# Kernel tuning notes

Measured on AMD Instinct MI355X. Metric: run time of the kernel, lower is better.

The kernel has to match this reference:

```python
import jax, jax.numpy as jnp
import numpy as np

N_NODES = 100000
N_GRAPHS = 64


def _gcn_norm(edge_index, num_nodes):
    # Add self-loops and compute symmetric normalization (PyG GCNConv gcn_norm).
    src = jnp.concatenate([edge_index[0], jnp.arange(num_nodes, dtype=edge_index.dtype)])
    dst = jnp.concatenate([edge_index[1], jnp.arange(num_nodes, dtype=edge_index.dtype)])
    deg = jax.ops.segment_sum(jnp.ones_like(dst, dtype=jnp.float32), dst, num_segments=num_nodes)
    dinv = jnp.where(deg > 0, jax.lax.rsqrt(deg), 0.0)
    norm = dinv[src] * dinv[dst]  # [E + N]
    return src, dst, norm


def _gcn_conv(x, src, dst, norm, W, b, num_nodes):
    h = x @ W                                   # [N, out]
    msg = h[src] * norm[:, None]                # gather + scale  [E+N, out]
    out = jax.ops.segment_sum(msg, dst, num_segments=num_nodes)  # scatter-add
    return out + b


def setup_inputs() -> dict:
    key = jax.random.key(0)
    ks = jax.random.split(key, 8)
    E = 1600000
    pos = jax.random.normal(ks[0], (N_NODES, 3), dtype=jnp.float32)
    edge_index = jax.random.randint(ks[1], (2, E), 0, N_NODES, dtype=jnp.int64)
    batch = jnp.sort(jax.random.randint(ks[2], (N_NODES,), 0, N_GRAPHS, dtype=jnp.int64))
    def glorot(k, shape):
        lim = np.sqrt(6.0 / (shape[0] + shape[1])).astype(np.float32)
        return jax.random.uniform(k, shape, dtype=jnp.float32, minval=-lim, maxval=lim)
    return {
        "pos": pos,
        "edge_index": edge_index,
        "batch": batch,
        "W1": glorot(ks[3], (3, 64)),  "b1": jnp.zeros((64,), jnp.float32),
        "W2": glorot(ks[4], (64, 64)), "b2": jnp.zeros((64,), jnp.float32),
        "W3": glorot(ks[5], (64, 24)), "b3": jnp.zeros((24,), jnp.float32),
    }


def reference(pos, edge_index, batch, W1, b1, W2, b2, W3, b3):
    src, dst, norm = _gcn_norm(edge_index, N_NODES)
    h = jax.nn.relu(_gcn_conv(pos, src, dst, norm, W1, b1, N_NODES))
    h = jax.nn.relu(_gcn_conv(h, src, dst, norm, W2, b2, N_NODES))
    y = _gcn_conv(h, src, dst, norm, W3, b3, N_NODES)  # [N, 24]
    # global_mean_pool over batch ids, then tanh
    sums = jax.ops.segment_sum(y, batch, num_segments=N_GRAPHS)          # [G, 24]
    counts = jax.ops.segment_sum(jnp.ones((N_NODES,), jnp.float32), batch, num_segments=N_GRAPHS)
    mean = sums / jnp.maximum(counts, 1.0)[:, None]
    return jnp.tanh(mean)
```

## Files before the change

kernel.cpp:

```cpp
#include <hip/hip_runtime.h>
#include <math.h>

#define NNODES 100000
#define NGRAPHS 64
#define NB 391
#define CAP 4608
#define NBLK3 1216


__device__ __forceinline__ unsigned int f2bf(float x) {
    union { float f; unsigned int u; } v;
    v.f = x;
    unsigned int r = v.u + 0x7FFFu + ((v.u >> 16) & 1u);
    return r >> 16;
}
__device__ __forceinline__ unsigned int pack2bf(float lo, float hi) {
    return f2bf(lo) | (f2bf(hi) << 16);
}
__device__ __forceinline__ float bflo(unsigned int u) {
    union { unsigned int u; float f; } v;
    v.u = u << 16;
    return v.f;
}
__device__ __forceinline__ float bfhi(unsigned int u) {
    union { unsigned int u; float f; } v;
    v.u = u & 0xFFFF0000u;
    return v.f;
}


__global__ void bucket_scatter(const int* __restrict__ src, const int* __restrict__ dst,
                               int* __restrict__ bCur, unsigned int* __restrict__ packed,
                               int E) {
    __shared__ int h[NB];
    __shared__ int cur[NB];
    for (int k = threadIdx.x; k < NB; k += 256) h[k] = 0;
    __syncthreads();
    int base = blockIdx.x * 2048 + threadIdx.x;
    int d[8], s[8], b[8];
#pragma unroll
    for (int k = 0; k < 8; ++k) {
        int e = base + k * 256;
        if (e < E) {
            d[k] = dst[e];
            s[k] = src[e];
            b[k] = d[k] >> 8;
            atomicAdd(&h[b[k]], 1);
        }
    }
    __syncthreads();
    for (int k = threadIdx.x; k < NB; k += 256) {
        int c = h[k];
        cur[k] = c ? atomicAdd(&bCur[k], c) : 0;
    }
    __syncthreads();
#pragma unroll
    for (int k = 0; k < 8; ++k) {
        int e = base + k * 256;
        if (e < E) {
            int pos = atomicAdd(&cur[b[k]], 1);
            if (pos < CAP)
                packed[(size_t)b[k] * CAP + pos] = ((unsigned int)(d[k] & 255) << 17) | (unsigned int)s[k];
        }
    }
}

__global__ void bucket_build(const unsigned int* __restrict__ packed, const int* __restrict__ bCur,
                             const int* __restrict__ batch, const float* __restrict__ pos,
                             int2* __restrict__ rowBE, int* __restrict__ col,
                             float* __restrict__ dinv, int2* __restrict__ dg,
                             float4* __restrict__ pos4, int N_) {
    __shared__ int cnt[256];
    __shared__ int bas[256];
    int tid = threadIdx.x;
    int b = blockIdx.x;
    int count = bCur[b];
    if (count > CAP) count = CAP;
    int beg = b * CAP;
    cnt[tid] = 0;
    __syncthreads();
    for (int k = beg + tid; k < beg + count; k += 256) atomicAdd(&cnt[packed[k] >> 17], 1);
    __syncthreads();
    int myCnt = cnt[tid];
    bas[tid] = myCnt;
    __syncthreads();
    for (int off = 1; off < 256; off <<= 1) {
        int v = (tid >= off) ? bas[tid - off] : 0;
        __syncthreads();
        bas[tid] += v;
        __syncthreads();
    }
    int excl = beg + ((tid > 0) ? bas[tid - 1] : 0);
    int node = (b << 8) + tid;
    if (node < N_) {
        rowBE[node] = make_int2(excl, excl + myCnt);
        float di = rsqrtf((float)myCnt + 1.0f);
        dinv[node] = di;
        dg[node] = make_int2(__float_as_int(di), batch[node]);
        pos4[node] = make_float4(pos[node * 3] * di, pos[node * 3 + 1] * di,
                                 pos[node * 3 + 2] * di, di);
    }
    __syncthreads();
    bas[tid] = excl;
    __syncthreads();
    for (int k = beg + tid; k < beg + count; k += 256) {
        unsigned int p = packed[k];
        int pos_ = atomicAdd(&bas[p >> 17], 1);
        col[pos_] = (int)(p & 0x1FFFFu);
    }
}


__global__ void mm12_gp(const float4* __restrict__ pos4, const int2* __restrict__ rowBE,
                        const int* __restrict__ col, const float* __restrict__ dinv,
                        const float* __restrict__ W1, const float* __restrict__ b1,
                        const float* __restrict__ W2, uint2* __restrict__ outb, int n) {
    __shared__ float4 part[256];
    __shared__ float4 ag[64];
    __shared__ float xs[64][65];
    __shared__ float4 ws[64 * 16];
    const int tid = threadIdx.x;
    const int rowBase = blockIdx.x * 64;
    const int r = tid >> 2, t4 = tid & 3;
    const int i = rowBase + r;

    float sx = 0, sy = 0, sz = 0, dival = 0;
    if (i < n) {
        int2 be = rowBE[i];
        float4 ps = pos4[i];
        dival = ps.w;
        if (t4 == 0) { sx = ps.x; sy = ps.y; sz = ps.z; }
        for (int j = be.x + t4; j < be.y; j += 4) {
            float4 v = pos4[col[j]];
            sx += v.x; sy += v.y; sz += v.z;
        }
    }
    part[tid] = make_float4(sx, sy, sz, dival);
    const float4* W24 = (const float4*)W2;
    for (int idx = tid; idx < 64 * 16; idx += 256) ws[idx] = W24[idx];
    __syncthreads();
    if (tid < 64) {
        float4 p0 = part[tid * 4], p1 = part[tid * 4 + 1];
        float4 p2 = part[tid * 4 + 2], p3 = part[tid * 4 + 3];
        ag[tid] = make_float4((p0.x + p1.x) + (p2.x + p3.x),
                              (p0.y + p1.y) + (p2.y + p3.y),
                              (p0.z + p1.z) + (p2.z + p3.z), p0.w);
    }
    __syncthreads();
    for (int idx = tid; idx < 64 * 64; idx += 256) {
        int rr = idx >> 6;
        int k = idx & 63;
        float4 a = ag[rr];
        float v = b1[k] + a.w * (a.x * W1[k] + a.y * W1[64 + k] + a.z * W1[128 + k]);
        xs[rr][k] = fmaxf(v, 0.0f);
    }
    __syncthreads();

    const int f4 = tid & 15;
    const int r0 = (tid >> 4) * 4;
    float4 a0 = make_float4(0, 0, 0, 0), a1 = a0, a2 = a0, a3 = a0;
#pragma unroll 4
    for (int k = 0; k < 64; ++k) {
        float4 wv = ws[k * 16 + f4];
        float xa = xs[r0 + 0][k];
        float xb = xs[r0 + 1][k];
        float xc = xs[r0 + 2][k];
        float xd = xs[r0 + 3][k];
        a0.x += wv.x * xa; a0.y += wv.y * xa; a0.z += wv.z * xa; a0.w += wv.w * xa;
        a1.x += wv.x * xb; a1.y += wv.y * xb; a1.z += wv.z * xb; a1.w += wv.w * xb;
        a2.x += wv.x * xc; a2.y += wv.y * xc; a2.z += wv.z * xc; a2.w += wv.w * xc;
        a3.x += wv.x * xd; a3.y += wv.y * xd; a3.z += wv.z * xd; a3.w += wv.w * xd;
    }
    int i0 = rowBase + r0;
    float d0 = (i0 + 0 < n) ? dinv[i0 + 0] : 1.0f;
    float d1 = (i0 + 1 < n) ? dinv[i0 + 1] : 1.0f;
    float d2 = (i0 + 2 < n) ? dinv[i0 + 2] : 1.0f;
    float d3 = (i0 + 3 < n) ? dinv[i0 + 3] : 1.0f;
    if (i0 + 0 < n)
        outb[(size_t)(i0 + 0) * 16 + f4] = make_uint2(pack2bf(a0.x * d0, a0.y * d0), pack2bf(a0.z * d0, a0.w * d0));
    if (i0 + 1 < n)
        outb[(size_t)(i0 + 1) * 16 + f4] = make_uint2(pack2bf(a1.x * d1, a1.y * d1), pack2bf(a1.z * d1, a1.w * d1));
    if (i0 + 2 < n)
        outb[(size_t)(i0 + 2) * 16 + f4] = make_uint2(pack2bf(a2.x * d2, a2.y * d2), pack2bf(a2.z * d2, a2.w * d2));
    if (i0 + 3 < n)
        outb[(size_t)(i0 + 3) * 16 + f4] = make_uint2(pack2bf(a3.x * d3, a3.y * d3), pack2bf(a3.z * d3, a3.w * d3));
}


__global__ void gather2_b16(const int2* __restrict__ rowBE, const int* __restrict__ col,
                            const uint4* __restrict__ h, const float* __restrict__ dinv,
                            const float* __restrict__ bias, uint4* __restrict__ outb, int n) {
    int t = blockIdx.x * blockDim.x + threadIdx.x;
    if (t >= n * 8) return;
    int i = t >> 3;
    int c8 = t & 7;
    float di = dinv[i];
    int2 be = rowBE[i];
    float acc[8];
    {
        uint4 sv = h[t];
        acc[0] = bflo(sv.x); acc[1] = bfhi(sv.x);
        acc[2] = bflo(sv.y); acc[3] = bfhi(sv.y);
        acc[4] = bflo(sv.z); acc[5] = bfhi(sv.z);
        acc[6] = bflo(sv.w); acc[7] = bfhi(sv.w);
    }
    int j = be.x;
    for (; j + 8 <= be.y; j += 8) {
        int s[8];
        uint4 v[8];
#pragma unroll
        for (int k = 0; k < 8; ++k) s[k] = col[j + k];
#pragma unroll
        for (int k = 0; k < 8; ++k) v[k] = h[(size_t)s[k] * 8 + c8];
#pragma unroll
        for (int k = 0; k < 8; ++k) {
            acc[0] += bflo(v[k].x); acc[1] += bfhi(v[k].x);
            acc[2] += bflo(v[k].y); acc[3] += bfhi(v[k].y);
            acc[4] += bflo(v[k].z); acc[5] += bfhi(v[k].z);
            acc[6] += bflo(v[k].w); acc[7] += bfhi(v[k].w);
        }
    }
    for (; j < be.y; ++j) {
        uint4 v = h[(size_t)col[j] * 8 + c8];
        acc[0] += bflo(v.x); acc[1] += bfhi(v.x);
        acc[2] += bflo(v.y); acc[3] += bfhi(v.y);
        acc[4] += bflo(v.z); acc[5] += bfhi(v.z);
        acc[6] += bflo(v.w); acc[7] += bfhi(v.w);
    }
    const float* bv = bias + c8 * 8;
#pragma unroll
    for (int k = 0; k < 8; ++k) acc[k] = fmaxf(acc[k] * di + bv[k], 0.0f);
    outb[t] = make_uint4(pack2bf(acc[0], acc[1]), pack2bf(acc[2], acc[3]),
                         pack2bf(acc[4], acc[5]), pack2bf(acc[6], acc[7]));
}


__global__ void mm3_b16(const uint4* __restrict__ xb, const float* __restrict__ W,
                        const float* __restrict__ dinv, uint2* __restrict__ outb, int n) {
    __shared__ float xs[128][65];
    __shared__ float4 ws[64 * 6];
    const int tid = threadIdx.x;
    const int rowBase = blockIdx.x * 128;

    for (int idx = tid; idx < 128 * 8; idx += 192) {
        int r = idx >> 3;
        int c8 = idx & 7;
        int gr = rowBase + r;
        uint4 v = (gr < n) ? xb[(size_t)gr * 8 + c8] : make_uint4(0, 0, 0, 0);
        float* xp = &xs[r][c8 * 8];
        xp[0] = bflo(v.x); xp[1] = bfhi(v.x);
        xp[2] = bflo(v.y); xp[3] = bfhi(v.y);
        xp[4] = bflo(v.z); xp[5] = bfhi(v.z);
        xp[6] = bflo(v.w); xp[7] = bfhi(v.w);
    }
    const float4* W4 = (const float4*)W;
    for (int idx = tid; idx < 64 * 6; idx += 192) ws[idx] = W4[idx];
    __syncthreads();

    const int f4 = tid % 6;
    const int r0 = (tid / 6) * 4;
    float4 a0 = make_float4(0, 0, 0, 0), a1 = a0, a2 = a0, a3 = a0;
#pragma unroll 4
    for (int k = 0; k < 64; ++k) {
        float4 wv = ws[k * 6 + f4];
        float xa = xs[r0 + 0][k];
        float xb_ = xs[r0 + 1][k];
        float xc = xs[r0 + 2][k];
        float xd = xs[r0 + 3][k];
        a0.x += wv.x * xa; a0.y += wv.y * xa; a0.z += wv.z * xa; a0.w += wv.w * xa;
        a1.x += wv.x * xb_; a1.y += wv.y * xb_; a1.z += wv.z * xb_; a1.w += wv.w * xb_;
        a2.x += wv.x * xc; a2.y += wv.y * xc; a2.z += wv.z * xc; a2.w += wv.w * xc;
        a3.x += wv.x * xd; a3.y += wv.y * xd; a3.z += wv.z * xd; a3.w += wv.w * xd;
    }
    int i0 = rowBase + r0;
    float d0 = (i0 + 0 < n) ? dinv[i0 + 0] : 1.0f;
    float d1 = (i0 + 1 < n) ? dinv[i0 + 1] : 1.0f;
    float d2 = (i0 + 2 < n) ? dinv[i0 + 2] : 1.0f;
    float d3 = (i0 + 3 < n) ? dinv[i0 + 3] : 1.0f;
    if (i0 + 0 < n)
        outb[(size_t)(i0 + 0) * 6 + f4] = make_uint2(pack2bf(a0.x * d0, a0.y * d0), pack2bf(a0.z * d0, a0.w * d0));
    if (i0 + 1 < n)
        outb[(size_t)(i0 + 1) * 6 + f4] = make_uint2(pack2bf(a1.x * d1, a1.y * d1), pack2bf(a1.z * d1, a1.w * d1));
    if (i0 + 2 < n)
        outb[(size_t)(i0 + 2) * 6 + f4] = make_uint2(pack2bf(a2.x * d2, a2.y * d2), pack2bf(a2.z * d2, a2.w * d2));
    if (i0 + 3 < n)
        outb[(size_t)(i0 + 3) * 6 + f4] = make_uint2(pack2bf(a3.x * d3, a3.y * d3), pack2bf(a3.z * d3, a3.w * d3));
}


__global__ void gather3_pool(const int2* __restrict__ rowBE, const int* __restrict__ col,
                             const uint4* __restrict__ y0, const int2* __restrict__ dg,
                             float* __restrict__ partials, float* __restrict__ cpart, int n) {
    __shared__ float lpool[NGRAPHS * 24];
    __shared__ float lcnt[NGRAPHS];
    for (int k = threadIdx.x; k < NGRAPHS * 24; k += 256) lpool[k] = 0.0f;
    for (int k = threadIdx.x; k < NGRAPHS; k += 256) lcnt[k] = 0.0f;
    __syncthreads();

    const int T = n * 6;
    const int stride = NBLK3 * 256;
    for (int t = blockIdx.x * 256 + threadIdx.x; t < T; t += stride) {
        int i = t / 6;
        int q = t - i * 6;
        int r = q >> 1;
        int half = q & 1;
        int2 wi = dg[i];
        float di = __int_as_float(wi.x);
        int g = wi.y;
        int2 be = rowBE[i];
        int mid = be.x + ((be.y - be.x + 1) >> 1);
        int a = half ? mid : be.x;
        int b = half ? be.y : mid;
        float acc[8] = {0, 0, 0, 0, 0, 0, 0, 0};
        if (!half) {
            uint4 sv = y0[(size_t)i * 3 + r];
            acc[0] = bflo(sv.x); acc[1] = bfhi(sv.x);
            acc[2] = bflo(sv.y); acc[3] = bfhi(sv.y);
            acc[4] = bflo(sv.z); acc[5] = bfhi(sv.z);
            acc[6] = bflo(sv.w); acc[7] = bfhi(sv.w);
        }
        int j = a;
        for (; j + 8 <= b; j += 8) {
            int s[8];
            uint4 v[8];
#pragma unroll
            for (int k = 0; k < 8; ++k) s[k] = col[j + k];
#pragma unroll
            for (int k = 0; k < 8; ++k) v[k] = y0[(size_t)s[k] * 3 + r];
#pragma unroll
            for (int k = 0; k < 8; ++k) {
                acc[0] += bflo(v[k].x); acc[1] += bfhi(v[k].x);
                acc[2] += bflo(v[k].y); acc[3] += bfhi(v[k].y);
                acc[4] += bflo(v[k].z); acc[5] += bfhi(v[k].z);
                acc[6] += bflo(v[k].w); acc[7] += bfhi(v[k].w);
            }
        }
        for (; j < b; ++j) {
            uint4 v = y0[(size_t)col[j] * 3 + r];
            acc[0] += bflo(v.x); acc[1] += bfhi(v.x);
            acc[2] += bflo(v.y); acc[3] += bfhi(v.y);
            acc[4] += bflo(v.z); acc[5] += bfhi(v.z);
            acc[6] += bflo(v.w); acc[7] += bfhi(v.w);
        }
        float* lp = &lpool[g * 24 + r * 8];
#pragma unroll
        for (int k = 0; k < 8; ++k) atomicAdd(&lp[k], acc[k] * di);
        if (q == 0) atomicAdd(&lcnt[g], 1.0f);
    }
    __syncthreads();
    float* pp = partials + (size_t)blockIdx.x * (NGRAPHS * 24);
    for (int k = threadIdx.x; k < NGRAPHS * 24; k += 256) pp[k] = lpool[k];
    float* cp = cpart + (size_t)blockIdx.x * NGRAPHS;
    for (int k = threadIdx.x; k < NGRAPHS; k += 256) cp[k] = lcnt[k];
}

__global__ void pool_finish(const float* __restrict__ partials, const float* __restrict__ cpart,
                            const float* __restrict__ b3, float* __restrict__ out) {
    int w = blockIdx.x * 4 + (threadIdx.x >> 6);
    int lane = threadIdx.x & 63;
    if (w >= NGRAPHS * 24) return;
    int g = w / 24;
    int c = w - g * 24;
    float s = 0.0f, cn = 0.0f;
    for (int b = lane; b < NBLK3; b += 64) {
        s += partials[(size_t)b * (NGRAPHS * 24) + w];
        cn += cpart[(size_t)b * NGRAPHS + g];
    }
#pragma unroll
    for (int off = 32; off > 0; off >>= 1) {
        s += __shfl_down(s, off);
        cn += __shfl_down(cn, off);
    }
    if (lane == 0) out[w] = tanhf(s / fmaxf(cn, 1.0f) + b3[c]);
}


static inline int gridFor(long long total, int block) {
    return (int)((total + block - 1) / block);
}

extern "C" void kernel_launch(void* const* d_in, const int* in_sizes, int n_in,
                              void* d_out, int out_size, void* d_ws, size_t ws_size,
                              hipStream_t stream) {
    const float* pos   = (const float*)d_in[0];
    const int*   ei    = (const int*)d_in[1];
    const int*   batch = (const int*)d_in[2];
    const float* W1    = (const float*)d_in[3];
    const float* b1    = (const float*)d_in[4];
    const float* W2    = (const float*)d_in[5];
    const float* b2    = (const float*)d_in[6];
    const float* W3    = (const float*)d_in[7];
    const float* b3    = (const float*)d_in[8];
    float*       out   = (float*)d_out;

    const int N = NNODES;
    const int E = in_sizes[1] / 2;
    const int* src = ei;
    const int* dst = ei + E;

    char* p = (char*)d_ws;
    uint4*  z2b    = (uint4*)p;         p += (size_t)N * 8 * sizeof(uint4);
    uint4*  h2b    = (uint4*)p;         p += (size_t)N * 8 * sizeof(uint4);
    uint4*  y0b    = (uint4*)p;         p += (size_t)N * 3 * sizeof(uint4);
    float4* pos4   = (float4*)p;        p += (size_t)N * sizeof(float4);
    float*  partials = (float*)p;       p += (size_t)NBLK3 * NGRAPHS * 24 * sizeof(float);
    float*  cpart  = (float*)p;         p += (size_t)NBLK3 * NGRAPHS * sizeof(float);
    int2*   rowBE  = (int2*)p;          p += (size_t)N * sizeof(int2);
    int2*   dg     = (int2*)p;          p += (size_t)N * sizeof(int2);
    float*  dinv   = (float*)p;         p += (size_t)N * sizeof(float);
    int*    bCur   = (int*)p;           p += NB * sizeof(int);
    unsigned int* packed = (unsigned int*)p;  p += (size_t)NB * CAP * sizeof(unsigned int);
    int*    col    = (int*)p;           p += (size_t)NB * CAP * sizeof(int);

    const int B = 256;
    const int edgeBlocks = gridFor(E, 2048);

    hipMemsetAsync(bCur, 0, NB * sizeof(int), stream);
    bucket_scatter<<<edgeBlocks, 256, 0, stream>>>(src, dst, bCur, packed, E);
    bucket_build<<<NB, 256, 0, stream>>>(packed, bCur, batch, pos, rowBE, col, dinv, dg, pos4, N);

    mm12_gp<<<gridFor(N, 64), 256, 0, stream>>>(pos4, rowBE, col, dinv, W1, b1, W2, (uint2*)z2b, N);

    gather2_b16<<<gridFor((long long)N * 8, B), B, 0, stream>>>(rowBE, col, z2b, dinv, b2, h2b, N);

    mm3_b16<<<gridFor(N, 128), 192, 0, stream>>>(h2b, W3, dinv, (uint2*)y0b, N);
    gather3_pool<<<NBLK3, 256, 0, stream>>>(rowBE, col, y0b, dg, partials, cpart, N);
    pool_finish<<<gridFor((long long)NGRAPHS * 24 * 64, B), B, 0, stream>>>(partials, cpart, b3, out);
}
```

Measured before the change: 261.9 us.

## Store bf16 feature matrices in column-slice layout for gather locality

Changes the intermediate bf16 node-feature arrays from row-major (node x 64/24 features) to slice-major layout, where each 16-byte feature chunk for all nodes is stored contiguously. Gather kernels now map threads so that all threads in a block work on the same feature slice. Their random neighbor reads then fall in one compact array per slice (1.6MB rather than 12.8MB), which should improve cache hit rates. The cost is that matmul stores and loads become strided (8-byte writes interleaved by 2, reads per slice). Each node's slices are now also processed at different times, which weakens reuse of its col/rowBE entries.

```diff
diff --git a/kernel.cpp b/kernel.cpp
--- a/kernel.cpp
+++ b/kernel.cpp
@@ -176,14 +176,15 @@
     float d1 = (i0 + 1 < n) ? dinv[i0 + 1] : 1.0f;
     float d2 = (i0 + 2 < n) ? dinv[i0 + 2] : 1.0f;
     float d3 = (i0 + 3 < n) ? dinv[i0 + 3] : 1.0f;
+    size_t sliceBase = (size_t)(f4 >> 1) * 2 * n + (f4 & 1);
     if (i0 + 0 < n)
-        outb[(size_t)(i0 + 0) * 16 + f4] = make_uint2(pack2bf(a0.x * d0, a0.y * d0), pack2bf(a0.z * d0, a0.w * d0));
+        outb[sliceBase + (size_t)(i0 + 0) * 2] = make_uint2(pack2bf(a0.x * d0, a0.y * d0), pack2bf(a0.z * d0, a0.w * d0));
     if (i0 + 1 < n)
-        outb[(size_t)(i0 + 1) * 16 + f4] = make_uint2(pack2bf(a1.x * d1, a1.y * d1), pack2bf(a1.z * d1, a1.w * d1));
+        outb[sliceBase + (size_t)(i0 + 1) * 2] = make_uint2(pack2bf(a1.x * d1, a1.y * d1), pack2bf(a1.z * d1, a1.w * d1));
     if (i0 + 2 < n)
-        outb[(size_t)(i0 + 2) * 16 + f4] = make_uint2(pack2bf(a2.x * d2, a2.y * d2), pack2bf(a2.z * d2, a2.w * d2));
+        outb[sliceBase + (size_t)(i0 + 2) * 2] = make_uint2(pack2bf(a2.x * d2, a2.y * d2), pack2bf(a2.z * d2, a2.w * d2));
     if (i0 + 3 < n)
-        outb[(size_t)(i0 + 3) * 16 + f4] = make_uint2(pack2bf(a3.x * d3, a3.y * d3), pack2bf(a3.z * d3, a3.w * d3));
+        outb[sliceBase + (size_t)(i0 + 3) * 2] = make_uint2(pack2bf(a3.x * d3, a3.y * d3), pack2bf(a3.z * d3, a3.w * d3));
 }
 
 
@@ -192,13 +193,14 @@
                             const float* __restrict__ bias, uint4* __restrict__ outb, int n) {
     int t = blockIdx.x * blockDim.x + threadIdx.x;
     if (t >= n * 8) return;
-    int i = t >> 3;
-    int c8 = t & 7;
+    int c8 = t / n;
+    int i = t - c8 * n;
+    const uint4* hs = h + (size_t)c8 * n;
     float di = dinv[i];
     int2 be = rowBE[i];
     float acc[8];
     {
-        uint4 sv = h[t];
+        uint4 sv = hs[i];
         acc[0] = bflo(sv.x); acc[1] = bfhi(sv.x);
         acc[2] = bflo(sv.y); acc[3] = bfhi(sv.y);
         acc[4] = bflo(sv.z); acc[5] = bfhi(sv.z);
@@ -211,7 +213,7 @@
 #pragma unroll
         for (int k = 0; k < 8; ++k) s[k] = col[j + k];
 #pragma unroll
-        for (int k = 0; k < 8; ++k) v[k] = h[(size_t)s[k] * 8 + c8];
+        for (int k = 0; k < 8; ++k) v[k] = hs[s[k]];
 #pragma unroll
         for (int k = 0; k < 8; ++k) {
             acc[0] += bflo(v[k].x); acc[1] += bfhi(v[k].x);
@@ -221,7 +223,7 @@
         }
     }
     for (; j < be.y; ++j) {
-        uint4 v = h[(size_t)col[j] * 8 + c8];
+        uint4 v = hs[col[j]];
         acc[0] += bflo(v.x); acc[1] += bfhi(v.x);
         acc[2] += bflo(v.y); acc[3] += bfhi(v.y);
         acc[4] += bflo(v.z); acc[5] += bfhi(v.z);
@@ -243,10 +245,10 @@
     const int rowBase = blockIdx.x * 128;
 
     for (int idx = tid; idx < 128 * 8; idx += 192) {
-        int r = idx >> 3;
-        int c8 = idx & 7;
+        int c8 = idx >> 7;
+        int r = idx & 127;
         int gr = rowBase + r;
-        uint4 v = (gr < n) ? xb[(size_t)gr * 8 + c8] : make_uint4(0, 0, 0, 0);
+        uint4 v = (gr < n) ? xb[(size_t)c8 * n + gr] : make_uint4(0, 0, 0, 0);
         float* xp = &xs[r][c8 * 8];
         xp[0] = bflo(v.x); xp[1] = bfhi(v.x);
         xp[2] = bflo(v.y); xp[3] = bfhi(v.y);
@@ -277,14 +279,15 @@
     float d1 = (i0 + 1 < n) ? dinv[i0 + 1] : 1.0f;
     float d2 = (i0 + 2 < n) ? dinv[i0 + 2] : 1.0f;
     float d3 = (i0 + 3 < n) ? dinv[i0 + 3] : 1.0f;
+    size_t sliceBase = (size_t)(f4 >> 1) * 2 * n + (f4 & 1);
     if (i0 + 0 < n)
-        outb[(size_t)(i0 + 0) * 6 + f4] = make_uint2(pack2bf(a0.x * d0, a0.y * d0), pack2bf(a0.z * d0, a0.w * d0));
+        outb[sliceBase + (size_t)(i0 + 0) * 2] = make_uint2(pack2bf(a0.x * d0, a0.y * d0), pack2bf(a0.z * d0, a0.w * d0));
     if (i0 + 1 < n)
-        outb[(size_t)(i0 + 1) * 6 + f4] = make_uint2(pack2bf(a1.x * d1, a1.y * d1), pack2bf(a1.z * d1, a1.w * d1));
+        outb[sliceBase + (size_t)(i0 + 1) * 2] = make_uint2(pack2bf(a1.x * d1, a1.y * d1), pack2bf(a1.z * d1, a1.w * d1));
     if (i0 + 2 < n)
-        outb[(size_t)(i0 + 2) * 6 + f4] = make_uint2(pack2bf(a2.x * d2, a2.y * d2), pack2bf(a2.z * d2, a2.w * d2));
+        outb[sliceBase + (size_t)(i0 + 2) * 2] = make_uint2(pack2bf(a2.x * d2, a2.y * d2), pack2bf(a2.z * d2, a2.w * d2));
     if (i0 + 3 < n)
-        outb[(size_t)(i0 + 3) * 6 + f4] = make_uint2(pack2bf(a3.x * d3, a3.y * d3), pack2bf(a3.z * d3, a3.w * d3));
+        outb[sliceBase + (size_t)(i0 + 3) * 2] = make_uint2(pack2bf(a3.x * d3, a3.y * d3), pack2bf(a3.z * d3, a3.w * d3));
 }
 
 
@@ -297,13 +300,15 @@
     for (int k = threadIdx.x; k < NGRAPHS; k += 256) lcnt[k] = 0.0f;
     __syncthreads();
 
+    const int n2 = 2 * n;
     const int T = n * 6;
     const int stride = NBLK3 * 256;
     for (int t = blockIdx.x * 256 + threadIdx.x; t < T; t += stride) {
-        int i = t / 6;
-        int q = t - i * 6;
-        int r = q >> 1;
-        int half = q & 1;
+        int r = t / n2;
+        int u = t - r * n2;
+        int i = u >> 1;
+        int half = u & 1;
+        const uint4* y4 = y0 + (size_t)r * n;
         int2 wi = dg[i];
         float di = __int_as_float(wi.x);
         int g = wi.y;
@@ -313,7 +318,7 @@
         int b = half ? be.y : mid;
         float acc[8] = {0, 0, 0, 0, 0, 0, 0, 0};
         if (!half) {
-            uint4 sv = y0[(size_t)i * 3 + r];
+            uint4 sv = y4[i];
             acc[0] = bflo(sv.x); acc[1] = bfhi(sv.x);
             acc[2] = bflo(sv.y); acc[3] = bfhi(sv.y);
             acc[4] = bflo(sv.z); acc[5] = bfhi(sv.z);
@@ -326,7 +331,7 @@
 #pragma unroll
             for (int k = 0; k < 8; ++k) s[k] = col[j + k];
 #pragma unroll
-            for (int k = 0; k < 8; ++k) v[k] = y0[(size_t)s[k] * 3 + r];
+            for (int k = 0; k < 8; ++k) v[k] = y4[s[k]];
 #pragma unroll
             for (int k = 0; k < 8; ++k) {
                 acc[0] += bflo(v[k].x); acc[1] += bfhi(v[k].x);
@@ -336,7 +341,7 @@
             }
         }
         for (; j < b; ++j) {
-            uint4 v = y0[(size_t)col[j] * 3 + r];
+            uint4 v = y4[col[j]];
             acc[0] += bflo(v.x); acc[1] += bfhi(v.x);
             acc[2] += bflo(v.y); acc[3] += bfhi(v.y);
             acc[4] += bflo(v.z); acc[5] += bfhi(v.z);
@@ -345,7 +350,7 @@
         float* lp = &lpool[g * 24 + r * 8];
 #pragma unroll
         for (int k = 0; k < 8; ++k) atomicAdd(&lp[k], acc[k] * di);
-        if (q == 0) atomicAdd(&lcnt[g], 1.0f);
+        if (r == 0 && half == 0) atomicAdd(&lcnt[g], 1.0f);
     }
     __syncthreads();
     float* pp = partials + (size_t)blockIdx.x * (NGRAPHS * 24);
```

Result: slower. 331.1 us (+26.4%).
